# Kernel optimization log

Measured on AMD Instinct MI355X. Metric: run time of the kernel, lower is better.

Reference implementation:

```python
import jax, jax.numpy as jnp
import numpy as np

H = 8          # num_heads
D = 256        # num_hiddens (left == right embed dim)
DH = D // H    # per-head dim
SH = 64        # num_attention_score_hiddens
B = 4
L_LEFT = 128
L_RIGHT = 256
NEG = -1e6


def _split_heads(x):
    # [B, L, D] -> [B*H, L, D/H]
    b, l, d = x.shape
    return x.reshape(b, l, H, d // H).transpose(0, 2, 1, 3).reshape(b * H, l, d // H)


def _merge_heads(x):
    # [B*H, L, dh] -> [B, L, H*dh]
    bh, l, dh = x.shape
    return x.reshape(-1, H, l, dh).transpose(0, 2, 1, 3).reshape(-1, l, H * dh)


def _additive_attention(q, k, v, valid, Wq, Wk, wv):
    # q: [BH, Lq, dh], k/v: [BH, Lk, dh], valid: [BH] int
    qf = q @ Wq                                   # [BH, Lq, SH]
    kf = k @ Wk                                   # [BH, Lk, SH]
    feats = jnp.tanh(qf[:, :, None, :] + kf[:, None, :, :])   # [BH, Lq, Lk, SH]
    scores = jnp.einsum('bqkh,h->bqk', feats, wv)              # [BH, Lq, Lk]
    lk = k.shape[1]
    mask = jnp.arange(lk)[None, None, :] < valid[:, None, None]
    scores = jnp.where(mask, scores, NEG)
    w = jax.nn.softmax(scores, axis=-1)
    return w @ v                                  # [BH, Lq, dh]


def setup_inputs() -> dict:
    key = jax.random.key(0)
    ks = jax.random.split(key, 16)
    f32 = jnp.float32
    s_w = 1.0 / np.sqrt(DH)
    s_v = 1.0 / np.sqrt(SH)
    s_o = 1.0 / np.sqrt(D)
    return {
        'queries_left': jax.random.normal(ks[0], (B, L_LEFT, D), f32),
        'keys_right':   jax.random.normal(ks[1], (B, L_RIGHT, D), f32),
        'values_right': jax.random.normal(ks[2], (B, L_RIGHT, D), f32),
        'queries_right': jax.random.normal(ks[3], (B, L_RIGHT, D), f32),
        'keys_left':    jax.random.normal(ks[4], (B, L_LEFT, D), f32),
        'values_left':  jax.random.normal(ks[5], (B, L_LEFT, D), f32),
        'Wq_l': jax.random.normal(ks[6], (DH, SH), f32) * s_w,
        'Wk_l': jax.random.normal(ks[7], (DH, SH), f32) * s_w,
        'wv_l': jax.random.normal(ks[8], (SH,), f32) * s_v,
        'Wo_l': jax.random.normal(ks[9], (D, D), f32) * s_o,
        'Wq_r': jax.random.normal(ks[10], (DH, SH), f32) * s_w,
        'Wk_r': jax.random.normal(ks[11], (DH, SH), f32) * s_w,
        'wv_r': jax.random.normal(ks[12], (SH,), f32) * s_v,
        'Wo_r': jax.random.normal(ks[13], (D, D), f32) * s_o,
        'valid_lens_right': jax.random.randint(ks[14], (B,), 1, L_RIGHT + 1).astype(jnp.int32),
        'valid_lens_left':  jax.random.randint(ks[15], (B,), 1, L_LEFT + 1).astype(jnp.int32),
    }


def reference(queries_left, keys_right, values_right, queries_right, keys_left,
              values_left, Wq_l, Wk_l, wv_l, Wo_l, Wq_r, Wk_r, wv_r, Wo_r,
              valid_lens_right, valid_lens_left):
    ql = _split_heads(queries_left)
    kr = _split_heads(keys_right)
    vr = _split_heads(values_right)
    qr = _split_heads(queries_right)
    kl = _split_heads(keys_left)
    vl = _split_heads(values_left)
    vlr = jnp.repeat(valid_lens_right, H)   # [B*H]
    vll = jnp.repeat(valid_lens_left, H)
    out_l = _additive_attention(ql, kr, vr, vlr, Wq_l, Wk_l, wv_l)
    out_r = _additive_attention(qr, kl, vl, vll, Wq_r, Wk_r, wv_r)
    out_l = _merge_heads(out_l) @ Wo_l      # [B, L_LEFT, D]
    out_r = _merge_heads(out_r) @ Wo_r      # [B, L_RIGHT, D]
    return out_l, out_r
```

## Files before the change

kernel.cpp:

```cpp
#include <hip/hip_runtime.h>
#include <math.h>


#define LOG2E 1.4426950408889634f
#define SCALE2 (2.0f * LOG2E)

#define OFF_QFL 0
#define OFF_KFL 262144
#define OFF_QFR 786432
#define OFF_KFR 1310720
#define OFF_HOL 1572864
#define OFF_HOR 1703936

static __device__ __forceinline__ float fast_exp2(float x) {
#if __has_builtin(__builtin_amdgcn_exp2f)
    return __builtin_amdgcn_exp2f(x);
#else
    return exp2f(x);
#endif
}

static __device__ __forceinline__ float fast_rcp(float x) {
#if __has_builtin(__builtin_amdgcn_rcpf)
    return __builtin_amdgcn_rcpf(x);
#else
    return 1.0f / x;
#endif
}

static __device__ __forceinline__ float sigm2(float x) {
    return fast_rcp(1.0f + fast_exp2(x));
}

__global__ __launch_bounds__(256) void k1_proj(
    const float* __restrict__ ql, const float* __restrict__ kr,
    const float* __restrict__ qr, const float* __restrict__ kl,
    const float* __restrict__ wql, const float* __restrict__ wkl,
    const float* __restrict__ wqr, const float* __restrict__ wkr,
    float* __restrict__ ws)
{
    int blk = blockIdx.x;
    const float* X; const float* W; float* out; int L; int ktype;
    if (blk < 256)       { X = ql; W = wql; out = ws + OFF_QFL; L = 128; ktype = 0; }
    else if (blk < 768)  { X = kr; W = wkl; out = ws + OFF_KFL; L = 256; ktype = 1; blk -= 256; }
    else if (blk < 1280) { X = qr; W = wqr; out = ws + OFF_QFR; L = 256; ktype = 0; blk -= 768; }
    else                 { X = kl; W = wkr; out = ws + OFF_KFR; L = 128; ktype = 1; blk -= 1280; }

    const int tiles = L >> 4;
    const int bh = blk / tiles;
    const int l0 = (blk - bh * tiles) << 4;
    const int b = bh >> 3, hd = bh & 7;
    const int t = threadIdx.x;
    const int h = t & 63, lsub = t >> 6;

    float wcol[32];
#pragma unroll
    for (int j = 0; j < 32; ++j) wcol[j] = W[j * 64 + h];

    const float* xb = X + ((b * L + l0 + lsub * 4) * 256) + hd * 32;

#pragma unroll
    for (int i = 0; i < 4; ++i) {
        const float4* xp = (const float4*)(xb + i * 256);
        float acc = 0.f;
#pragma unroll
        for (int j4 = 0; j4 < 8; ++j4) {
            float4 a = xp[j4];
            acc += a.x * wcol[4 * j4 + 0];
            acc += a.y * wcol[4 * j4 + 1];
            acc += a.z * wcol[4 * j4 + 2];
            acc += a.w * wcol[4 * j4 + 3];
        }
        acc *= SCALE2;
        const int l = l0 + lsub * 4 + i;
        if (!ktype) out[(bh * L + l) * 64 + h] = acc;
        else        out[bh * (L * 64) + (h >> 2) * (L * 4) + l * 4 + (h & 3)] = acc;
    }
}

template<int LK, int LQ, int TQ>
__device__ __forceinline__ void attn_side(
    int bh, int q0,
    const float* qf, const float* kf4,
    const float* __restrict__ wv, const float* __restrict__ v,
    const int* __restrict__ vlen, float* ho,
    float* s_lds, float* pv_lds, float* c_lds)
{
    constexpr int G   = 256 / LK;
    constexpr int RPT = TQ / G;
    const int t = threadIdx.x;

    if (t < 64) c_lds[t] = wv[t] * (-2.0f * LOG2E);
    __syncthreads();

    const int k = t & (LK - 1);
    const int g = (LK == 256) ? 0 : (t >> 7);
    const int b = bh >> 3, hd = bh & 7;
    const int valid = vlen[b];

    float acc[RPT];
#pragma unroll
    for (int r = 0; r < RPT; ++r) acc[r] = 0.f;

    if ((k & ~63) < valid) {
        const float* kfp = kf4 + bh * (64 * LK) + k * 4;
        const float* qfp = qf + (bh * LQ + q0 + g * RPT) * 64;
#pragma unroll 4
        for (int hc = 0; hc < 16; ++hc) {
            const float4 kv = *(const float4*)(kfp + hc * (LK * 4));
            const float4 cv = *(const float4*)(c_lds + hc * 4);
#pragma unroll
            for (int r = 0; r < RPT; ++r) {
                const float4 qv = *(const float4*)(qfp + r * 64 + hc * 4);
                acc[r] += cv.x * sigm2(qv.x + kv.x);
                acc[r] += cv.y * sigm2(qv.y + kv.y);
                acc[r] += cv.z * sigm2(qv.z + kv.z);
                acc[r] += cv.w * sigm2(qv.w + kv.w);
            }
        }
    }
#pragma unroll
    for (int r = 0; r < RPT; ++r) {
        const int row = g * RPT + r;
        s_lds[row * LK + k] = (k < valid) ? acc[r] : -1.0e6f;
    }
    __syncthreads();

    {
        const int wid = t >> 6, lane = t & 63;
        constexpr int RPW = TQ / 4;
        constexpr int CPL = LK / 64;
#pragma unroll
        for (int rr = 0; rr < RPW; ++rr) {
            const int row = wid * RPW + rr;
            float sv[CPL];
            float m = -3.0e38f;
#pragma unroll
            for (int j = 0; j < CPL; ++j) {
                sv[j] = s_lds[row * LK + lane + 64 * j];
                m = fmaxf(m, sv[j]);
            }
#pragma unroll
            for (int off = 1; off < 64; off <<= 1) m = fmaxf(m, __shfl_xor(m, off));
            float lsum = 0.f;
#pragma unroll
            for (int j = 0; j < CPL; ++j) { sv[j] = fast_exp2(sv[j] - m); lsum += sv[j]; }
#pragma unroll
            for (int off = 1; off < 64; off <<= 1) lsum += __shfl_xor(lsum, off);
            const float inv = fast_rcp(lsum);
#pragma unroll
            for (int j = 0; j < CPL; ++j) s_lds[row * LK + lane + 64 * j] = sv[j] * inv;
        }
    }
    __syncthreads();

    {
        const int d = t & 31, kc = t >> 5;
        constexpr int CS = LK / 8;
        if (kc * CS < valid) {
            float vv[CS];
            const float* vp = v + (b * LK + kc * CS) * 256 + hd * 32 + d;
#pragma unroll
            for (int i = 0; i < CS; ++i) vv[i] = vp[i * 256];
#pragma unroll
            for (int row = 0; row < TQ; ++row) {
                const float4* pp = (const float4*)(s_lds + row * LK + kc * CS);
                float a = 0.f;
#pragma unroll
                for (int i4 = 0; i4 < CS / 4; ++i4) {
                    float4 p = pp[i4];
                    a += p.x * vv[4 * i4 + 0];
                    a += p.y * vv[4 * i4 + 1];
                    a += p.z * vv[4 * i4 + 2];
                    a += p.w * vv[4 * i4 + 3];
                }
                pv_lds[(kc * TQ + row) * 32 + d] = a;
            }
        } else {
#pragma unroll
            for (int row = 0; row < TQ; ++row) pv_lds[(kc * TQ + row) * 32 + d] = 0.f;
        }
    }
    __syncthreads();

    if (t < TQ * 32) {
        const int dd = t & 31, row = t >> 5;
        float o = 0.f;
#pragma unroll
        for (int kc2 = 0; kc2 < 8; ++kc2) o += pv_lds[(kc2 * TQ + row) * 32 + dd];
        ho[(b * LQ + q0 + row) * 256 + hd * 32 + dd] = o;
    }
}

__global__ __launch_bounds__(256) void k2_attn(
    float* ws,
    const float* __restrict__ wvl, const float* __restrict__ wvr,
    const float* __restrict__ vr, const float* __restrict__ vl,
    const int* __restrict__ vlr, const int* __restrict__ vll)
{
    __shared__ __align__(16) float s_lds[1024];
    __shared__ __align__(16) float pv_lds[2048];
    __shared__ __align__(16) float c_lds[64];
    int blk = blockIdx.x;
    if (blk < 1024) {
        const int bh = blk >> 5, q0 = (blk & 31) << 2;
        attn_side<256, 128, 4>(bh, q0, ws + OFF_QFL, ws + OFF_KFL, wvl, vr, vlr,
                               ws + OFF_HOL, s_lds, pv_lds, c_lds);
    } else {
        blk -= 1024;
        const int bh = blk >> 5, q0 = (blk & 31) << 3;
        attn_side<128, 256, 8>(bh, q0, ws + OFF_QFR, ws + OFF_KFR, wvr, vl, vll,
                               ws + OFF_HOR, s_lds, pv_lds, c_lds);
    }
}

__global__ __launch_bounds__(256) void k3_proj(
    const float* ws,
    const float* __restrict__ wol, const float* __restrict__ wor,
    float* __restrict__ out)
{
    __shared__ __align__(16) float a_lds[1024];
    const int row0 = blockIdx.x * 4;
    const float* A; const float* W; float* op; int lr0;
    if (row0 < 512) { A = ws + OFF_HOL; W = wol; op = out;          lr0 = row0; }
    else            { A = ws + OFF_HOR; W = wor; op = out + 131072; lr0 = row0 - 512; }

    const int t = threadIdx.x;
#pragma unroll
    for (int i = 0; i < 4; ++i) a_lds[i * 256 + t] = A[(lr0 + i) * 256 + t];
    __syncthreads();

    float acc[4];
#pragma unroll
    for (int r = 0; r < 4; ++r) acc[r] = 0.f;

#pragma unroll 4
    for (int k4 = 0; k4 < 64; ++k4) {
        const float w0 = W[(k4 * 4 + 0) * 256 + t];
        const float w1 = W[(k4 * 4 + 1) * 256 + t];
        const float w2 = W[(k4 * 4 + 2) * 256 + t];
        const float w3 = W[(k4 * 4 + 3) * 256 + t];
#pragma unroll
        for (int r = 0; r < 4; ++r) {
            const float4 a = *(const float4*)(a_lds + r * 256 + k4 * 4);
            acc[r] += a.x * w0 + a.y * w1 + a.z * w2 + a.w * w3;
        }
    }
#pragma unroll
    for (int r = 0; r < 4; ++r) op[(lr0 + r) * 256 + t] = acc[r];
}

extern "C" void kernel_launch(void* const* d_in, const int* in_sizes, int n_in,
                              void* d_out, int out_size, void* d_ws, size_t ws_size,
                              hipStream_t stream)
{
    const float* ql  = (const float*)d_in[0];
    const float* kr  = (const float*)d_in[1];
    const float* vr  = (const float*)d_in[2];
    const float* qr  = (const float*)d_in[3];
    const float* kl  = (const float*)d_in[4];
    const float* vl  = (const float*)d_in[5];
    const float* wql = (const float*)d_in[6];
    const float* wkl = (const float*)d_in[7];
    const float* wvl = (const float*)d_in[8];
    const float* wol = (const float*)d_in[9];
    const float* wqr = (const float*)d_in[10];
    const float* wkr = (const float*)d_in[11];
    const float* wvr = (const float*)d_in[12];
    const float* wor = (const float*)d_in[13];
    const int*   vlr = (const int*)d_in[14];
    const int*   vll = (const int*)d_in[15];
    float* ws  = (float*)d_ws;
    float* out = (float*)d_out;

    hipLaunchKernelGGL(k1_proj, dim3(1536), dim3(256), 0, stream,
                       ql, kr, qr, kl, wql, wkl, wqr, wkr, ws);
    hipLaunchKernelGGL(k2_attn, dim3(2048), dim3(256), 0, stream,
                       ws, wvl, wvr, vr, vl, vlr, vll);
    hipLaunchKernelGGL(k3_proj, dim3(384), dim3(256), 0, stream,
                       ws, wol, wor, out);
}
```

Baseline: 134.3 us.

## Factor tanh via exp products and split attention into scores and PV kernels

The projection kernel now stores exp(2x) of the query and key features, so tanh(q+k) can be built from a product eq*ek+1 instead of an exp per element. Pairs of rows share one reciprocal, which cuts transcendental work in the score loop. The fused attention kernel is split into a scores-plus-softmax kernel that writes the probability matrix to global memory and a separate PV kernel. The cost is an extra launch and a global round trip for P, plus a risk of overflow in exp for large projections.

```diff
diff --git a/kernel.cpp b/kernel.cpp
--- a/kernel.cpp
+++ b/kernel.cpp
@@ -4,13 +4,16 @@
 
 #define LOG2E 1.4426950408889634f
 #define SCALE2 (2.0f * LOG2E)
-
-#define OFF_QFL 0
-#define OFF_KFL 262144
-#define OFF_QFR 786432
-#define OFF_KFR 1310720
-#define OFF_HOL 1572864
-#define OFF_HOR 1703936
+#define NEGS  (-2.0f * LOG2E)
+
+#define OFF_EQL 0
+#define OFF_EKL 262144
+#define OFF_EQR 786432
+#define OFF_EKR 1310720
+#define OFF_PL  1572864
+#define OFF_PR  2621440
+#define OFF_HOL 3670016
+#define OFF_HOR 3801088
 
 static __device__ __forceinline__ float fast_exp2(float x) {
 #if __has_builtin(__builtin_amdgcn_exp2f)
@@ -19,7 +22,6 @@
     return exp2f(x);
 #endif
 }
-
 static __device__ __forceinline__ float fast_rcp(float x) {
 #if __has_builtin(__builtin_amdgcn_rcpf)
     return __builtin_amdgcn_rcpf(x);
@@ -28,10 +30,6 @@
 #endif
 }
 
-static __device__ __forceinline__ float sigm2(float x) {
-    return fast_rcp(1.0f + fast_exp2(x));
-}
-
 __global__ __launch_bounds__(256) void k1_proj(
     const float* __restrict__ ql, const float* __restrict__ kr,
     const float* __restrict__ qr, const float* __restrict__ kl,
@@ -39,12 +37,13 @@
     const float* __restrict__ wqr, const float* __restrict__ wkr,
     float* __restrict__ ws)
 {
+    __shared__ float tlds[64 * 17];
     int blk = blockIdx.x;
     const float* X; const float* W; float* out; int L; int ktype;
-    if (blk < 256)       { X = ql; W = wql; out = ws + OFF_QFL; L = 128; ktype = 0; }
-    else if (blk < 768)  { X = kr; W = wkl; out = ws + OFF_KFL; L = 256; ktype = 1; blk -= 256; }
-    else if (blk < 1280) { X = qr; W = wqr; out = ws + OFF_QFR; L = 256; ktype = 0; blk -= 768; }
-    else                 { X = kl; W = wkr; out = ws + OFF_KFR; L = 128; ktype = 1; blk -= 1280; }
+    if (blk < 256)       { X = ql; W = wql; out = ws + OFF_EQL; L = 128; ktype = 0; }
+    else if (blk < 768)  { X = kr; W = wkl; out = ws + OFF_EKL; L = 256; ktype = 1; blk -= 256; }
+    else if (blk < 1280) { X = qr; W = wqr; out = ws + OFF_EQR; L = 256; ktype = 0; blk -= 768; }
+    else                 { X = kl; W = wkr; out = ws + OFF_EKR; L = 128; ktype = 1; blk -= 1280; }
 
     const int tiles = L >> 4;
     const int bh = blk / tiles;
@@ -71,151 +70,174 @@
             acc += a.z * wcol[4 * j4 + 2];
             acc += a.w * wcol[4 * j4 + 3];
         }
-        acc *= SCALE2;
-        const int l = l0 + lsub * 4 + i;
-        if (!ktype) out[(bh * L + l) * 64 + h] = acc;
-        else        out[bh * (L * 64) + (h >> 2) * (L * 4) + l * 4 + (h & 3)] = acc;
-    }
-}
-
-template<int LK, int LQ, int TQ>
-__device__ __forceinline__ void attn_side(
-    int bh, int q0,
-    const float* qf, const float* kf4,
-    const float* __restrict__ wv, const float* __restrict__ v,
-    const int* __restrict__ vlen, float* ho,
-    float* s_lds, float* pv_lds, float* c_lds)
-{
-    constexpr int G   = 256 / LK;
-    constexpr int RPT = TQ / G;
+        const float e = fast_exp2(acc * SCALE2);
+        const int lloc = lsub * 4 + i;
+        if (!ktype) out[(bh * L + l0 + lloc) * 64 + h] = e;
+        else        tlds[h * 17 + lloc] = e;
+    }
+    if (ktype) {
+        __syncthreads();
+        const int ll = t & 15, hq = t >> 4;
+#pragma unroll
+        for (int hh = 0; hh < 4; ++hh) {
+            const int h2 = hq + 16 * hh;
+            out[bh * (64 * L) + h2 * L + l0 + ll] = tlds[h2 * 17 + ll];
+        }
+    }
+}
+
+template<int LK, int LQ, int RPT, int J>
+static __device__ __forceinline__ void scores_side(
+    int bh, int row0,
+    const float* __restrict__ eq, const float* __restrict__ ek,
+    const float* __restrict__ wv, int valid, float* __restrict__ P)
+{
+    const int lane = threadIdx.x & 63;
+    float acc[RPT][J];
+#pragma unroll
+    for (int r = 0; r < RPT; ++r)
+#pragma unroll
+        for (int j = 0; j < J; ++j) acc[r][j] = 0.f;
+
+    const float* ekb = ek + bh * (64 * LK) + lane;
+    const float* eqb = eq + (bh * LQ + row0) * 64;
+
+#pragma unroll
+    for (int j = 0; j < J; ++j) {
+        if (64 * j < valid) {
+#pragma unroll
+            for (int hc = 0; hc < 16; ++hc) {
+                const float4 wv4 = *(const float4*)(wv + hc * 4);
+                float wva[4] = {wv4.x, wv4.y, wv4.z, wv4.w};
+                float eqa[RPT][4];
+#pragma unroll
+                for (int r = 0; r < RPT; ++r) {
+                    const float4 q4 = *(const float4*)(eqb + r * 64 + hc * 4);
+                    eqa[r][0] = q4.x; eqa[r][1] = q4.y; eqa[r][2] = q4.z; eqa[r][3] = q4.w;
+                }
+#pragma unroll
+                for (int hs = 0; hs < 4; ++hs) {
+                    const float ekv = ekb[(hc * 4 + hs) * LK + 64 * j];
+#pragma unroll
+                    for (int pr = 0; pr < RPT / 2; ++pr) {
+                        const float d0 = fmaf(eqa[2 * pr    ][hs], ekv, 1.0f);
+                        const float d1 = fmaf(eqa[2 * pr + 1][hs], ekv, 1.0f);
+                        const float rr = fast_rcp(d0 * d1);
+                        acc[2 * pr    ][j] += (wva[hs] * d1) * rr;
+                        acc[2 * pr + 1][j] += (wva[hs] * d0) * rr;
+                    }
+                }
+            }
+        }
+    }
+
+#pragma unroll
+    for (int r = 0; r < RPT; ++r) {
+        float sv[J];
+        float m = -3.0e38f;
+#pragma unroll
+        for (int j = 0; j < J; ++j) {
+            sv[j] = (64 * j + lane < valid) ? acc[r][j] * NEGS : -1.0e6f;
+            m = fmaxf(m, sv[j]);
+        }
+#pragma unroll
+        for (int off = 1; off < 64; off <<= 1) m = fmaxf(m, __shfl_xor(m, off));
+        float lsum = 0.f;
+#pragma unroll
+        for (int j = 0; j < J; ++j) { sv[j] = fast_exp2(sv[j] - m); lsum += sv[j]; }
+#pragma unroll
+        for (int off = 1; off < 64; off <<= 1) lsum += __shfl_xor(lsum, off);
+        const float inv = fast_rcp(lsum);
+        float* pp = P + (bh * LQ + row0 + r) * LK + lane;
+#pragma unroll
+        for (int j = 0; j < J; ++j) pp[64 * j] = sv[j] * inv;
+    }
+}
+
+__global__ __launch_bounds__(256) void k2a_scores(
+    const float* __restrict__ eql, const float* __restrict__ ekl,
+    const float* __restrict__ eqr, const float* __restrict__ ekr,
+    const float* __restrict__ wvl, const float* __restrict__ wvr,
+    const int* __restrict__ vlr, const int* __restrict__ vll,
+    float* __restrict__ pl, float* __restrict__ pr)
+{
+    const int w = threadIdx.x >> 6;
+    int blk = blockIdx.x;
+    if (blk < 512) {
+        const int bh = blk >> 4, q0 = (blk & 15) << 3;
+        scores_side<256, 128, 2, 4>(bh, q0 + 2 * w, eql, ekl, wvl,
+                                    vlr[bh >> 3], pl);
+    } else {
+        blk -= 512;
+        const int bh = blk >> 4, q0 = (blk & 15) << 4;
+        scores_side<128, 256, 4, 2>(bh, q0 + 4 * w, eqr, ekr, wvr,
+                                    vll[bh >> 3], pr);
+    }
+}
+
+template<int LK, int LQ>
+static __device__ __forceinline__ void pv_side(
+    int bh, int q0, const float* __restrict__ P,
+    const float* __restrict__ v, int valid,
+    float* __restrict__ ho, float* pv_lds)
+{
+    constexpr int TQ = 8, CS = LK / 8;
     const int t = threadIdx.x;
-
-    if (t < 64) c_lds[t] = wv[t] * (-2.0f * LOG2E);
+    const int d = t & 31, kc = t >> 5;
+    const int b = bh >> 3, hd = bh & 7;
+
+    if (kc * CS < valid) {
+        float vv[CS];
+        const float* vp = v + (b * LK + kc * CS) * 256 + hd * 32 + d;
+#pragma unroll
+        for (int i = 0; i < CS; ++i) vv[i] = vp[i * 256];
+#pragma unroll
+        for (int row = 0; row < TQ; ++row) {
+            const float4* pp = (const float4*)(P + (bh * LQ + q0 + row) * LK + kc * CS);
+            float a = 0.f;
+#pragma unroll
+            for (int i4 = 0; i4 < CS / 4; ++i4) {
+                float4 p = pp[i4];
+                a += p.x * vv[4 * i4 + 0];
+                a += p.y * vv[4 * i4 + 1];
+                a += p.z * vv[4 * i4 + 2];
+                a += p.w * vv[4 * i4 + 3];
+            }
+            pv_lds[(kc * TQ + row) * 32 + d] = a;
+        }
+    } else {
+#pragma unroll
+        for (int row = 0; row < TQ; ++row) pv_lds[(kc * TQ + row) * 32 + d] = 0.f;
+    }
     __syncthreads();
 
-    const int k = t & (LK - 1);
-    const int g = (LK == 256) ? 0 : (t >> 7);
-    const int b = bh >> 3, hd = bh & 7;
-    const int valid = vlen[b];
-
-    float acc[RPT];
-#pragma unroll
-    for (int r = 0; r < RPT; ++r) acc[r] = 0.f;
-
-    if ((k & ~63) < valid) {
-        const float* kfp = kf4 + bh * (64 * LK) + k * 4;
-        const float* qfp = qf + (bh * LQ + q0 + g * RPT) * 64;
-#pragma unroll 4
-        for (int hc = 0; hc < 16; ++hc) {
-            const float4 kv = *(const float4*)(kfp + hc * (LK * 4));
-            const float4 cv = *(const float4*)(c_lds + hc * 4);
-#pragma unroll
-            for (int r = 0; r < RPT; ++r) {
-                const float4 qv = *(const float4*)(qfp + r * 64 + hc * 4);
-                acc[r] += cv.x * sigm2(qv.x + kv.x);
-                acc[r] += cv.y * sigm2(qv.y + kv.y);
-                acc[r] += cv.z * sigm2(qv.z + kv.z);
-                acc[r] += cv.w * sigm2(qv.w + kv.w);
-            }
-        }
-    }
-#pragma unroll
-    for (int r = 0; r < RPT; ++r) {
-        const int row = g * RPT + r;
-        s_lds[row * LK + k] = (k < valid) ? acc[r] : -1.0e6f;
-    }
-    __syncthreads();
-
-    {
-        const int wid = t >> 6, lane = t & 63;
-        constexpr int RPW = TQ / 4;
-        constexpr int CPL = LK / 64;
-#pragma unroll
-        for (int rr = 0; rr < RPW; ++rr) {
-            const int row = wid * RPW + rr;
-            float sv[CPL];
-            float m = -3.0e38f;
-#pragma unroll
-            for (int j = 0; j < CPL; ++j) {
-                sv[j] = s_lds[row * LK + lane + 64 * j];
-                m = fmaxf(m, sv[j]);
-            }
-#pragma unroll
-            for (int off = 1; off < 64; off <<= 1) m = fmaxf(m, __shfl_xor(m, off));
-            float lsum = 0.f;
-#pragma unroll
-            for (int j = 0; j < CPL; ++j) { sv[j] = fast_exp2(sv[j] - m); lsum += sv[j]; }
-#pragma unroll
-            for (int off = 1; off < 64; off <<= 1) lsum += __shfl_xor(lsum, off);
-            const float inv = fast_rcp(lsum);
-#pragma unroll
-            for (int j = 0; j < CPL; ++j) s_lds[row * LK + lane + 64 * j] = sv[j] * inv;
-        }
-    }
-    __syncthreads();
-
-    {
-        const int d = t & 31, kc = t >> 5;
-        constexpr int CS = LK / 8;
-        if (kc * CS < valid) {
-            float vv[CS];
-            const float* vp = v + (b * LK + kc * CS) * 256 + hd * 32 + d;
-#pragma unroll
-            for (int i = 0; i < CS; ++i) vv[i] = vp[i * 256];
-#pragma unroll
-            for (int row = 0; row < TQ; ++row) {
-                const float4* pp = (const float4*)(s_lds + row * LK + kc * CS);
-                float a = 0.f;
-#pragma unroll
-                for (int i4 = 0; i4 < CS / 4; ++i4) {
-                    float4 p = pp[i4];
-                    a += p.x * vv[4 * i4 + 0];
-                    a += p.y * vv[4 * i4 + 1];
-                    a += p.z * vv[4 * i4 + 2];
-                    a += p.w * vv[4 * i4 + 3];
-                }
-                pv_lds[(kc * TQ + row) * 32 + d] = a;
-            }
-        } else {
-#pragma unroll
-            for (int row = 0; row < TQ; ++row) pv_lds[(kc * TQ + row) * 32 + d] = 0.f;
-        }
-    }
-    __syncthreads();
-
-    if (t < TQ * 32) {
-        const int dd = t & 31, row = t >> 5;
-        float o = 0.f;
-#pragma unroll
-        for (int kc2 = 0; kc2 < 8; ++kc2) o += pv_lds[(kc2 * TQ + row) * 32 + dd];
-        ho[(b * LQ + q0 + row) * 256 + hd * 32 + dd] = o;
-    }
-}
-
-__global__ __launch_bounds__(256) void k2_attn(
-    float* ws,
-    const float* __restrict__ wvl, const float* __restrict__ wvr,
+    const int dd = t & 31, row = t >> 5;
+    float o = 0.f;
+#pragma unroll
+    for (int kc2 = 0; kc2 < 8; ++kc2) o += pv_lds[(kc2 * TQ + row) * 32 + dd];
+    ho[(b * LQ + q0 + row) * 256 + hd * 32 + dd] = o;
+}
+
+__global__ __launch_bounds__(256) void k2b_pv(
+    const float* __restrict__ pl, const float* __restrict__ pr,
     const float* __restrict__ vr, const float* __restrict__ vl,
-    const int* __restrict__ vlr, const int* __restrict__ vll)
-{
-    __shared__ __align__(16) float s_lds[1024];
+    const int* __restrict__ vlr, const int* __restrict__ vll,
+    float* __restrict__ hol, float* __restrict__ hor)
+{
     __shared__ __align__(16) float pv_lds[2048];
-    __shared__ __align__(16) float c_lds[64];
     int blk = blockIdx.x;
-    if (blk < 1024) {
-        const int bh = blk >> 5, q0 = (blk & 31) << 2;
-        attn_side<256, 128, 4>(bh, q0, ws + OFF_QFL, ws + OFF_KFL, wvl, vr, vlr,
-                               ws + OFF_HOL, s_lds, pv_lds, c_lds);
+    if (blk < 512) {
+        const int bh = blk >> 4, q0 = (blk & 15) << 3;
+        pv_side<256, 128>(bh, q0, pl, vr, vlr[bh >> 3], hol, pv_lds);
     } else {
-        blk -= 1024;
+        blk -= 512;
         const int bh = blk >> 5, q0 = (blk & 31) << 3;
-        attn_side<128, 256, 8>(bh, q0, ws + OFF_QFR, ws + OFF_KFR, wvr, vl, vll,
-                               ws + OFF_HOR, s_lds, pv_lds, c_lds);
+        pv_side<128, 256>(bh, q0, pr, vl, vll[bh >> 3], hor, pv_lds);
     }
 }
 
 __global__ __launch_bounds__(256) void k3_proj(
-    const float* ws,
+    const float* __restrict__ ws,
     const float* __restrict__ wol, const float* __restrict__ wor,
     float* __restrict__ out)
 {
@@ -275,8 +297,12 @@
 
     hipLaunchKernelGGL(k1_proj, dim3(1536), dim3(256), 0, stream,
                        ql, kr, qr, kl, wql, wkl, wqr, wkr, ws);
-    hipLaunchKernelGGL(k2_attn, dim3(2048), dim3(256), 0, stream,
-                       ws, wvl, wvr, vr, vl, vlr, vll);
+    hipLaunchKernelGGL(k2a_scores, dim3(1024), dim3(256), 0, stream,
+                       ws + OFF_EQL, ws + OFF_EKL, ws + OFF_EQR, ws + OFF_EKR,
+                       wvl, wvr, vlr, vll, ws + OFF_PL, ws + OFF_PR);
+    hipLaunchKernelGGL(k2b_pv, dim3(1536), dim3(256), 0, stream,
+                       ws + OFF_PL, ws + OFF_PR, vr, vl, vlr, vll,
+                       ws + OFF_HOL, ws + OFF_HOR);
     hipLaunchKernelGGL(k3_proj, dim3(384), dim3(256), 0, stream,
                        ws, wol, wor, out);
 }
```

Measured after the change: 134.3 us. No clear change (-0.0%).
